# Kernel tuning notes

Measured on AMD Instinct MI355X. Metric: run time of the kernel, lower is better.

## Reference

```python
import jax, jax.numpy as jnp
import numpy as np

H = 1024        # hidden_size
E = 16          # n_routed_experts
K = 4           # num_experts_per_tok (top_k)
I = 512         # moe_intermediate_size
NS = 2          # n_shared_experts
IS = I * NS     # shared-expert intermediate size
N = 2048        # num_tokens
ROUTED_SCALE = 2.5  # routed_scaling_factor


def setup_inputs() -> dict:
    key = jax.random.key(0)
    ks = jax.random.split(key, 6)
    s = 0.02
    return {
        "hidden_states": jax.random.normal(ks[0], (N, H), jnp.float32),
        "gate_w": jax.random.normal(ks[1], (H, E), jnp.float32) * s,
        "w_gate_up": jax.random.normal(ks[2], (E, H, 2 * I), jnp.float32) * s,
        "w_down": jax.random.normal(ks[3], (E, I, H), jnp.float32) * s,
        "shared_gate_up": jax.random.normal(ks[4], (H, 2 * IS), jnp.float32) * s,
        "shared_down": jax.random.normal(ks[5], (IS, H), jnp.float32) * s,
    }


def _moe_forward(x, gate_w, w_gate_up, w_down, shared_gate_up, shared_down):
    n = x.shape[0]
    # --- router: sigmoid scoring + top-k (num_expert_group=topk_group=1) ---
    router_logits = x @ gate_w                      # [N, E]
    scores = jax.nn.sigmoid(router_logits)
    top_vals, top_idx = jax.lax.top_k(scores, K)    # [N, K]
    # renormalize (norm_topk_prob=True)
    top_w = top_vals / jnp.sum(top_vals, axis=-1, keepdims=True)
    # dense combine weights [N, E], zero outside top-k
    w_dense = jnp.zeros((n, E), x.dtype).at[jnp.arange(n)[:, None], top_idx].add(top_w)

    # --- routed experts: SwiGLU per expert, weighted combine ---
    gu = jnp.einsum("nh,ehf->nef", x, w_gate_up)    # [N, E, 2I]
    act = jax.nn.silu(gu[..., :I]) * gu[..., I:]    # SiluAndMul -> [N, E, I]
    routed = jnp.einsum("nei,eih,ne->nh", act, w_down, w_dense)  # [N, H]

    # --- shared experts MLP (WBLMLP) ---
    gus = x @ shared_gate_up                        # [N, 2*IS]
    shared = (jax.nn.silu(gus[:, :IS]) * gus[:, IS:]) @ shared_down  # [N, H]

    return routed * ROUTED_SCALE + shared


def reference(hidden_states, gate_w, w_gate_up, w_down, shared_gate_up, shared_down):
    return _moe_forward(hidden_states, gate_w, w_gate_up, w_down,
                        shared_gate_up, shared_down)
```

## Files before the change

### kernel.cpp

```cpp
#include <hip/hip_runtime.h>
#include <hip/hip_bf16.h>
#include <stdint.h>

#define NTOK 2048
#define HDIM 1024
#define NEXP 16
#define TOPK 4
#define IR   512
#define ISH  1024
#define RSCALE 2.5f

typedef short bf16x4 __attribute__((ext_vector_type(4)));
typedef short bf16x8 __attribute__((ext_vector_type(8)));
typedef float f32x4  __attribute__((ext_vector_type(4)));

static __device__ __forceinline__ unsigned short f2bf(float f){
  union { float fv; uint32_t u; } v; v.fv = f;
  uint32_t r = v.u + 0x7fffu + ((v.u >> 16) & 1u);
  return (unsigned short)(r >> 16);
}
static __device__ __forceinline__ float bf2f(unsigned short s){
  union { uint32_t u; float f; } v; v.u = ((uint32_t)s) << 16;
  return v.f;
}

static __device__ __forceinline__ void gl_lds16(const void* gp, void* lp){
  __builtin_amdgcn_global_load_lds(
      (const __attribute__((address_space(1))) unsigned int*)gp,
      (__attribute__((address_space(3))) unsigned int*)lp, 16, 0, 0);
}

__global__ __launch_bounds__(256) void router_kernel(
    const float* __restrict__ x, const float* __restrict__ gw,
    float* __restrict__ topkw, int* __restrict__ choice,
    unsigned short* __restrict__ xbf)
{
  __shared__ float sgw[NEXP][HDIM + 8];
  const int tid = threadIdx.x;
  for (int f = tid; f < HDIM * NEXP; f += 256){
    int i = f >> 4, e = f & 15;
    sgw[e][i] = gw[f];
  }
  __syncthreads();
  const int lane = tid & 63;
  const int t = blockIdx.x * 4 + (tid >> 6);

  float s[NEXP];
  #pragma unroll
  for (int e = 0; e < NEXP; e++) s[e] = 0.f;
  #pragma unroll
  for (int j = 0; j < 8; j++){
    const int off = 128 * j + lane * 2;
    float2 xv = *(const float2*)(x + (size_t)t * HDIM + off);
    ushort2 xs = { f2bf(xv.x), f2bf(xv.y) };
    *(ushort2*)(xbf + (size_t)t * HDIM + off) = xs;
    #pragma unroll
    for (int e = 0; e < NEXP; e++){
      float2 gv = *(const float2*)(&sgw[e][off]);
      s[e] += xv.x * gv.x + xv.y * gv.y;
    }
  }
  #pragma unroll
  for (int e = 0; e < NEXP; e++){
    #pragma unroll
    for (int off = 32; off; off >>= 1)
      s[e] += __shfl_xor(s[e], off);
  }
  float sc[NEXP];
  #pragma unroll
  for (int e = 0; e < NEXP; e++) sc[e] = 1.f / (1.f + __expf(-s[e]));

  unsigned mask = 0; float w[TOPK]; int id[TOPK];
  #pragma unroll
  for (int k = 0; k < TOPK; k++){
    float best = -1e30f; int bi = 0;
    #pragma unroll
    for (int e = 0; e < NEXP; e++){
      if (!((mask >> e) & 1u) && sc[e] > best){ best = sc[e]; bi = e; }
    }
    mask |= 1u << bi; id[k] = bi; w[k] = best;
  }
  float inv = 1.f / (w[0] + w[1] + w[2] + w[3]);
  if (lane == 0){
    #pragma unroll
    for (int k = 0; k < TOPK; k++){
      topkw[t * TOPK + k] = w[k] * inv;
      choice[t * TOPK + k] = id[k];
    }
  }
}

__global__ __launch_bounds__(256) void build_lists(
    const int* __restrict__ choice, int* __restrict__ counts, int* __restrict__ lists)
{
  const int e = blockIdx.x;
  const int tid = threadIdx.x;
  __shared__ int scnt[256];
  const int base = tid * 32;
  unsigned m = 0; int local = 0;
  #pragma unroll
  for (int i = 0; i < 32; i++){
    bool hit = (choice[base + i] == e);
    m |= (unsigned)hit << i;
    local += hit;
  }
  scnt[tid] = local;
  __syncthreads();
  int v = local;
  for (int off = 1; off < 256; off <<= 1){
    int add = (tid >= off) ? scnt[tid - off] : 0;
    __syncthreads();
    v += add; scnt[tid] = v;
    __syncthreads();
  }
  int pos = v - local;
  #pragma unroll
  for (int i = 0; i < 32; i++){
    if ((m >> i) & 1u) lists[e * NTOK + pos++] = base + i;
  }
  if (tid == 255) counts[e] = v;
}

__global__ __launch_bounds__(256) void gu_gemm(
    const unsigned short* __restrict__ xbf, const float* __restrict__ wgu,
    const float* __restrict__ sgu,
    unsigned short* __restrict__ act_r, unsigned short* __restrict__ act_s,
    const int* __restrict__ lists, const int* __restrict__ counts)
{
  __shared__ unsigned short sA[128 * 64];
  __shared__ unsigned short sB[128 * 64];
  __shared__ int sAid[128];

  const int tid = threadIdx.x;
  const int L = blockIdx.x;
  const bool routed = (L < 512);
  int e, mIdx, n0, count, NPAIR, NCH, LDB;
  const float* Bsrc;
  unsigned short* act;
  if (routed){
    e = L >> 5; int r = L & 31; mIdx = r >> 3; n0 = (r & 7) * 64;
    count = counts[e]; NPAIR = IR; NCH = 4; LDB = 2 * IR;
    Bsrc = wgu + (size_t)e * HDIM * (2 * IR);
    act = act_r;
  } else {
    int v = L - 512;
    e = 0; mIdx = v >> 4; n0 = (v & 15) * 64;
    count = NTOK; NPAIR = ISH; NCH = 16; LDB = 2 * ISH;
    Bsrc = sgu; act = act_s;
  }

  const int wv = tid >> 6, lane = tid & 63, lr = lane & 15, g = lane >> 4;
  const int wm = wv >> 1, wn = wv & 1;

  const int a = tid & 31, o = tid >> 5;
  const int alo = a & 15, aup = a >> 4;
  const int grp = ((alo >> 3) << 1) | aup;
  const int cbase = grp * 32 + 4 * (alo & 7);
  const int bsw = alo & 7;
  const int gcol = n0 + 4 * alo + (aup ? NPAIR : 0);
  const float* bthread = Bsrc + (size_t)(o * 8) * LDB + gcol;

  for (int mt = mIdx; mt * 128 < count; mt += NCH){
    const int m0 = mt * 128;
    __syncthreads();
    if (tid < 128){
      int idx = m0 + tid;
      int aid;
      if (routed) aid = (idx < count) ? lists[e * NTOK + idx] : lists[e * NTOK];
      else        aid = idx;
      sAid[tid] = aid;
    }
    __syncthreads();
    const unsigned short* asrc[4];
    #pragma unroll
    for (int it = 0; it < 4; it++){
      int s = tid + it * 256;
      int row = s >> 3, ch = s & 7;
      int aid = sAid[row];
      int tok = routed ? (aid >> 2) : aid;
      asrc[it] = xbf + (size_t)tok * HDIM + ch * 8;
    }

    const f32x4 z4 = {0.f, 0.f, 0.f, 0.f};
    f32x4 acc[4][4];
    #pragma unroll
    for (int i = 0; i < 4; i++)
      #pragma unroll
      for (int j = 0; j < 4; j++) acc[i][j] = z4;

    for (int k0 = 0; k0 < HDIM; k0 += 64){
      #pragma unroll
      for (int it = 0; it < 4; it++)
        gl_lds16(asrc[it] + k0, sA + (tid + it * 256) * 8);
      float4 f[8];
      const float* bp = bthread + (size_t)k0 * LDB;
      #pragma unroll
      for (int r = 0; r < 8; r++)
        f[r] = *(const float4*)(bp + (size_t)r * LDB);
      #pragma unroll
      for (int i = 0; i < 4; i++){
        const float* fp0 = (const float*)&f[0];
        bf16x8 pk = { (short)f2bf(((const float*)&f[0])[i]), (short)f2bf(((const float*)&f[1])[i]),
                      (short)f2bf(((const float*)&f[2])[i]), (short)f2bf(((const float*)&f[3])[i]),
                      (short)f2bf(((const float*)&f[4])[i]), (short)f2bf(((const float*)&f[5])[i]),
                      (short)f2bf(((const float*)&f[6])[i]), (short)f2bf(((const float*)&f[7])[i]) };
        (void)fp0;
        int c = cbase + i;
        *(bf16x8*)(sB + c * 64 + ((o ^ bsw) << 3)) = pk;
      }
      __syncthreads();
      #pragma unroll
      for (int h = 0; h < 2; h++){
        bf16x8 af[4], bfr[4];
        #pragma unroll
        for (int i = 0; i < 4; i++)
          af[i] = *(const bf16x8*)(sA + (wm * 64 + i * 16 + lr) * 64 + h * 32 + g * 8);
        #pragma unroll
        for (int i = 0; i < 4; i++){
          int c = wn * 64 + i * 16 + lr;
          int pos = (h * 4 + g) ^ ((c >> 2) & 7);
          bfr[i] = *(const bf16x8*)(sB + c * 64 + pos * 8);
        }
        #pragma unroll
        for (int mi = 0; mi < 4; mi++)
          #pragma unroll
          for (int ni = 0; ni < 4; ni++)
            acc[mi][ni] = __builtin_amdgcn_mfma_f32_16x16x32_bf16(af[mi], bfr[ni], acc[mi][ni], 0, 0, 0);
      }
      __syncthreads();
    }

    #pragma unroll
    for (int mi = 0; mi < 4; mi++){
      #pragma unroll
      for (int r = 0; r < 4; r++){
        int row = wm * 64 + mi * 16 + g * 4 + r;
        if (routed && m0 + row >= count) continue;
        int aid = sAid[row];
        size_t arow = (size_t)aid * NPAIR;
        #pragma unroll
        for (int ni = 0; ni < 2; ni++){
          float gv = acc[mi][ni][r];
          float uv = acc[mi][ni + 2][r];
          float av = gv / (1.f + __expf(-gv)) * uv;
          act[arow + n0 + wn * 32 + ni * 16 + lr] = f2bf(av);
        }
      }
    }
  }
}

__global__ __launch_bounds__(256) void down_gemm(
    const unsigned short* __restrict__ act_r, const unsigned short* __restrict__ act_s,
    const float* __restrict__ wdn, const float* __restrict__ sdn,
    float* __restrict__ out, unsigned short* __restrict__ downout,
    const int* __restrict__ lists, const int* __restrict__ counts)
{
  __shared__ unsigned short sA[128 * 64];
  __shared__ unsigned short sB[128 * 64];
  __shared__ int sAid[128];

  const int tid = threadIdx.x;
  const int L = blockIdx.x;
  const bool routed = (L < 512);
  int e, mIdx, n0, count, K, NCH;
  const float* Bsrc;
  const unsigned short* Ab;
  if (routed){
    e = L >> 5; int r = L & 31; mIdx = r >> 3; n0 = (r & 7) * 128;
    count = counts[e]; K = IR; NCH = 4;
    Bsrc = wdn + (size_t)e * IR * HDIM;
    Ab = act_r;
  } else {
    int v = L - 512;
    e = 0; mIdx = v >> 3; n0 = (v & 7) * 128;
    count = NTOK; K = ISH; NCH = 16;
    Bsrc = sdn; Ab = act_s;
  }

  const int wv = tid >> 6, lane = tid & 63, lr = lane & 15, g = lane >> 4;
  const int wm = wv >> 1, wn = wv & 1;

  const int a = tid & 31, o = tid >> 5;
  const int cbase = 4 * a;
  const int bsw = a & 7;
  const float* bthread = Bsrc + (size_t)(o * 8) * HDIM + n0 + 4 * a;

  for (int mt = mIdx; mt * 128 < count; mt += NCH){
    const int m0 = mt * 128;
    __syncthreads();
    if (tid < 128){
      int idx = m0 + tid;
      int aid;
      if (routed) aid = (idx < count) ? lists[e * NTOK + idx] : lists[e * NTOK];
      else        aid = idx;
      sAid[tid] = aid;
    }
    __syncthreads();
    const unsigned short* asrc[4];
    #pragma unroll
    for (int it = 0; it < 4; it++){
      int s = tid + it * 256;
      int row = s >> 3, ch = s & 7;
      asrc[it] = Ab + (size_t)sAid[row] * K + ch * 8;
    }

    const f32x4 z4 = {0.f, 0.f, 0.f, 0.f};
    f32x4 acc[4][4];
    #pragma unroll
    for (int i = 0; i < 4; i++)
      #pragma unroll
      for (int j = 0; j < 4; j++) acc[i][j] = z4;

    for (int k0 = 0; k0 < K; k0 += 64){
      #pragma unroll
      for (int it = 0; it < 4; it++)
        gl_lds16(asrc[it] + k0, sA + (tid + it * 256) * 8);
      float4 f[8];
      const float* bp = bthread + (size_t)k0 * HDIM;
      #pragma unroll
      for (int r = 0; r < 8; r++)
        f[r] = *(const float4*)(bp + (size_t)r * HDIM);
      #pragma unroll
      for (int i = 0; i < 4; i++){
        bf16x8 pk = { (short)f2bf(((const float*)&f[0])[i]), (short)f2bf(((const float*)&f[1])[i]),
                      (short)f2bf(((const float*)&f[2])[i]), (short)f2bf(((const float*)&f[3])[i]),
                      (short)f2bf(((const float*)&f[4])[i]), (short)f2bf(((const float*)&f[5])[i]),
                      (short)f2bf(((const float*)&f[6])[i]), (short)f2bf(((const float*)&f[7])[i]) };
        int c = cbase + i;
        *(bf16x8*)(sB + c * 64 + ((o ^ bsw) << 3)) = pk;
      }
      __syncthreads();
      #pragma unroll
      for (int h = 0; h < 2; h++){
        bf16x8 af[4], bfr[4];
        #pragma unroll
        for (int i = 0; i < 4; i++)
          af[i] = *(const bf16x8*)(sA + (wm * 64 + i * 16 + lr) * 64 + h * 32 + g * 8);
        #pragma unroll
        for (int i = 0; i < 4; i++){
          int c = wn * 64 + i * 16 + lr;
          int pos = (h * 4 + g) ^ ((c >> 2) & 7);
          bfr[i] = *(const bf16x8*)(sB + c * 64 + pos * 8);
        }
        #pragma unroll
        for (int mi = 0; mi < 4; mi++)
          #pragma unroll
          for (int ni = 0; ni < 4; ni++)
            acc[mi][ni] = __builtin_amdgcn_mfma_f32_16x16x32_bf16(af[mi], bfr[ni], acc[mi][ni], 0, 0, 0);
      }
      __syncthreads();
    }

    #pragma unroll
    for (int mi = 0; mi < 4; mi++){
      #pragma unroll
      for (int r = 0; r < 4; r++){
        int row = wm * 64 + mi * 16 + g * 4 + r;
        if (m0 + row >= count) continue;
        int aid = sAid[row];
        size_t orow = (size_t)aid * HDIM;
        if (routed){
          #pragma unroll
          for (int ni = 0; ni < 4; ni++)
            downout[orow + n0 + wn * 64 + ni * 16 + lr] = f2bf(acc[mi][ni][r]);
        } else {
          #pragma unroll
          for (int ni = 0; ni < 4; ni++)
            out[orow + n0 + wn * 64 + ni * 16 + lr] = acc[mi][ni][r];
        }
      }
    }
  }
}

__global__ __launch_bounds__(256) void combine_kernel(
    float* __restrict__ out, const unsigned short* __restrict__ downout,
    const float* __restrict__ topkw)
{
  const int idx = blockIdx.x * 256 + threadIdx.x;
  const int t = idx >> 8;
  const int c4 = (idx & 255) * 4;
  float4 o = *(float4*)(out + (size_t)t * HDIM + c4);
  float r0 = 0.f, r1 = 0.f, r2 = 0.f, r3 = 0.f;
  #pragma unroll
  for (int k = 0; k < TOPK; k++){
    float w = topkw[t * TOPK + k];
    const ushort4 dv = *(const ushort4*)(downout + (size_t)(t * TOPK + k) * HDIM + c4);
    r0 += w * bf2f(dv.x); r1 += w * bf2f(dv.y);
    r2 += w * bf2f(dv.z); r3 += w * bf2f(dv.w);
  }
  o.x += RSCALE * r0; o.y += RSCALE * r1; o.z += RSCALE * r2; o.w += RSCALE * r3;
  *(float4*)(out + (size_t)t * HDIM + c4) = o;
}

extern "C" void kernel_launch(void* const* d_in, const int* in_sizes, int n_in,
                              void* d_out, int out_size, void* d_ws, size_t ws_size,
                              hipStream_t stream) {
  const float* x   = (const float*)d_in[0];
  const float* gw  = (const float*)d_in[1];
  const float* wgu = (const float*)d_in[2];
  const float* wdn = (const float*)d_in[3];
  const float* sgu = (const float*)d_in[4];
  const float* sdn = (const float*)d_in[5];
  float* out = (float*)d_out;

  char* ws = (char*)d_ws;
  float* topkw = (float*)(ws + 0);
  int* choice  = (int*)(ws + 32768);
  int* counts  = (int*)(ws + 65536);
  int* lists   = (int*)(ws + 65792);
  unsigned short* xbf     = (unsigned short*)(ws + 197120);
  unsigned short* act_r   = (unsigned short*)(ws + 197120 +  4194304ull);
  unsigned short* act_s   = (unsigned short*)(ws + 197120 + 12582912ull);
  unsigned short* downout = (unsigned short*)(ws + 197120 + 16777216ull);

  router_kernel<<<NTOK / 4, 256, 0, stream>>>(x, gw, topkw, choice, xbf);
  build_lists<<<NEXP, 256, 0, stream>>>(choice, counts, lists);
  gu_gemm<<<768, 256, 0, stream>>>(xbf, wgu, sgu, act_r, act_s, lists, counts);
  down_gemm<<<640, 256, 0, stream>>>(act_r, act_s, wdn, sdn, out, downout, lists, counts);
  combine_kernel<<<(NTOK * HDIM / 4) / 256, 256, 0, stream>>>(out, downout, topkw);
}
```

Measured before the change: 141.5 us.

## Replace LDS-direct loads with register staging and XOR-swizzled LDS layout

```diff
diff --git a/kernel.cpp b/kernel.cpp
--- a/kernel.cpp
+++ b/kernel.cpp
@@ -23,11 +23,10 @@
   union { uint32_t u; float f; } v; v.u = ((uint32_t)s) << 16;
   return v.f;
 }
-
-static __device__ __forceinline__ void gl_lds16(const void* gp, void* lp){
-  __builtin_amdgcn_global_load_lds(
-      (const __attribute__((address_space(1))) unsigned int*)gp,
-      (__attribute__((address_space(3))) unsigned int*)lp, 16, 0, 0);
+static __device__ __forceinline__ unsigned int pkbf2(float lo, float hi){
+  union { __hip_bfloat162 b; unsigned int u; } cv;
+  cv.b = __float22bfloat162_rn(make_float2(lo, hi));
+  return cv.u;
 }
 
 __global__ __launch_bounds__(256) void router_kernel(
@@ -151,12 +150,12 @@
 
   const int wv = tid >> 6, lane = tid & 63, lr = lane & 15, g = lane >> 4;
   const int wm = wv >> 1, wn = wv & 1;
+  const int sw = lr >> 1;
 
   const int a = tid & 31, o = tid >> 5;
   const int alo = a & 15, aup = a >> 4;
   const int grp = ((alo >> 3) << 1) | aup;
   const int cbase = grp * 32 + 4 * (alo & 7);
-  const int bsw = alo & 7;
   const int gcol = n0 + 4 * alo + (aup ? NPAIR : 0);
   const float* bthread = Bsrc + (size_t)(o * 8) * LDB + gcol;
 
@@ -172,13 +171,15 @@
     }
     __syncthreads();
     const unsigned short* asrc[4];
+    unsigned short* adst[4];
     #pragma unroll
     for (int it = 0; it < 4; it++){
       int s = tid + it * 256;
-      int row = s >> 3, ch = s & 7;
+      int row = s >> 3, j = s & 7;
       int aid = sAid[row];
       int tok = routed ? (aid >> 2) : aid;
-      asrc[it] = xbf + (size_t)tok * HDIM + ch * 8;
+      asrc[it] = xbf + (size_t)tok * HDIM + j * 8;
+      adst[it] = sA + row * 64 + (j ^ ((row >> 1) & 7)) * 8;
     }
 
     const f32x4 z4 = {0.f, 0.f, 0.f, 0.f};
@@ -189,9 +190,13 @@
       for (int j = 0; j < 4; j++) acc[i][j] = z4;
 
     for (int k0 = 0; k0 < HDIM; k0 += 64){
+      bf16x8 av[4];
       #pragma unroll
       for (int it = 0; it < 4; it++)
-        gl_lds16(asrc[it] + k0, sA + (tid + it * 256) * 8);
+        av[it] = *(const bf16x8*)(asrc[it] + k0);
+      #pragma unroll
+      for (int it = 0; it < 4; it++)
+        *(bf16x8*)adst[it] = av[it];
       float4 f[8];
       const float* bp = bthread + (size_t)k0 * LDB;
       #pragma unroll
@@ -199,27 +204,26 @@
         f[r] = *(const float4*)(bp + (size_t)r * LDB);
       #pragma unroll
       for (int i = 0; i < 4; i++){
-        const float* fp0 = (const float*)&f[0];
-        bf16x8 pk = { (short)f2bf(((const float*)&f[0])[i]), (short)f2bf(((const float*)&f[1])[i]),
-                      (short)f2bf(((const float*)&f[2])[i]), (short)f2bf(((const float*)&f[3])[i]),
-                      (short)f2bf(((const float*)&f[4])[i]), (short)f2bf(((const float*)&f[5])[i]),
-                      (short)f2bf(((const float*)&f[6])[i]), (short)f2bf(((const float*)&f[7])[i]) };
-        (void)fp0;
+        union { bf16x8 v; unsigned int u[4]; } pk;
+        #pragma unroll
+        for (int rp = 0; rp < 4; rp++){
+          float lo = ((const float*)&f[2 * rp    ])[i];
+          float hi = ((const float*)&f[2 * rp + 1])[i];
+          pk.u[rp] = pkbf2(lo, hi);
+        }
         int c = cbase + i;
-        *(bf16x8*)(sB + c * 64 + ((o ^ bsw) << 3)) = pk;
+        int pos = o ^ ((c >> 1) & 7);
+        *(bf16x8*)(sB + c * 64 + pos * 8) = pk.v;
       }
       __syncthreads();
       #pragma unroll
       for (int h = 0; h < 2; h++){
         bf16x8 af[4], bfr[4];
         #pragma unroll
-        for (int i = 0; i < 4; i++)
-          af[i] = *(const bf16x8*)(sA + (wm * 64 + i * 16 + lr) * 64 + h * 32 + g * 8);
-        #pragma unroll
         for (int i = 0; i < 4; i++){
-          int c = wn * 64 + i * 16 + lr;
-          int pos = (h * 4 + g) ^ ((c >> 2) & 7);
-          bfr[i] = *(const bf16x8*)(sB + c * 64 + pos * 8);
+          int jx = ((h * 4 + g) ^ sw) * 8;
+          af[i]  = *(const bf16x8*)(sA + (wm * 64 + i * 16 + lr) * 64 + jx);
+          bfr[i] = *(const bf16x8*)(sB + (wn * 64 + i * 16 + lr) * 64 + jx);
         }
         #pragma unroll
         for (int mi = 0; mi < 4; mi++)
@@ -242,8 +246,8 @@
         for (int ni = 0; ni < 2; ni++){
           float gv = acc[mi][ni][r];
           float uv = acc[mi][ni + 2][r];
-          float av = gv / (1.f + __expf(-gv)) * uv;
-          act[arow + n0 + wn * 32 + ni * 16 + lr] = f2bf(av);
+          float av2 = gv / (1.f + __expf(-gv)) * uv;
+          act[arow + n0 + wn * 32 + ni * 16 + lr] = f2bf(av2);
         }
       }
     }
@@ -253,7 +257,7 @@
 __global__ __launch_bounds__(256) void down_gemm(
     const unsigned short* __restrict__ act_r, const unsigned short* __restrict__ act_s,
     const float* __restrict__ wdn, const float* __restrict__ sdn,
-    float* __restrict__ out, unsigned short* __restrict__ downout,
+    float* __restrict__ shout, unsigned short* __restrict__ downout,
     const int* __restrict__ lists, const int* __restrict__ counts)
 {
   __shared__ unsigned short sA[128 * 64];
@@ -280,10 +284,10 @@
 
   const int wv = tid >> 6, lane = tid & 63, lr = lane & 15, g = lane >> 4;
   const int wm = wv >> 1, wn = wv & 1;
+  const int sw = lr >> 1;
 
   const int a = tid & 31, o = tid >> 5;
   const int cbase = 4 * a;
-  const int bsw = a & 7;
   const float* bthread = Bsrc + (size_t)(o * 8) * HDIM + n0 + 4 * a;
 
   for (int mt = mIdx; mt * 128 < count; mt += NCH){
@@ -298,11 +302,13 @@
     }
     __syncthreads();
     const unsigned short* asrc[4];
+    unsigned short* adst[4];
     #pragma unroll
     for (int it = 0; it < 4; it++){
       int s = tid + it * 256;
-      int row = s >> 3, ch = s & 7;
-      asrc[it] = Ab + (size_t)sAid[row] * K + ch * 8;
+      int row = s >> 3, j = s & 7;
+      asrc[it] = Ab + (size_t)sAid[row] * K + j * 8;
+      adst[it] = sA + row * 64 + (j ^ ((row >> 1) & 7)) * 8;
     }
 
     const f32x4 z4 = {0.f, 0.f, 0.f, 0.f};
@@ -313,9 +319,13 @@
       for (int j = 0; j < 4; j++) acc[i][j] = z4;
 
     for (int k0 = 0; k0 < K; k0 += 64){
+      bf16x8 av[4];
       #pragma unroll
       for (int it = 0; it < 4; it++)
-        gl_lds16(asrc[it] + k0, sA + (tid + it * 256) * 8);
+        av[it] = *(const bf16x8*)(asrc[it] + k0);
+      #pragma unroll
+      for (int it = 0; it < 4; it++)
+        *(bf16x8*)adst[it] = av[it];
       float4 f[8];
       const float* bp = bthread + (size_t)k0 * HDIM;
       #pragma unroll
@@ -323,25 +333,26 @@
         f[r] = *(const float4*)(bp + (size_t)r * HDIM);
       #pragma unroll
       for (int i = 0; i < 4; i++){
-        bf16x8 pk = { (short)f2bf(((const float*)&f[0])[i]), (short)f2bf(((const float*)&f[1])[i]),
-                      (short)f2bf(((const float*)&f[2])[i]), (short)f2bf(((const float*)&f[3])[i]),
-                      (short)f2bf(((const float*)&f[4])[i]), (short)f2bf(((const float*)&f[5])[i]),
-                      (short)f2bf(((const float*)&f[6])[i]), (short)f2bf(((const float*)&f[7])[i]) };
+        union { bf16x8 v; unsigned int u[4]; } pk;
+        #pragma unroll
+        for (int rp = 0; rp < 4; rp++){
+          float lo = ((const float*)&f[2 * rp    ])[i];
+          float hi = ((const float*)&f[2 * rp + 1])[i];
+          pk.u[rp] = pkbf2(lo, hi);
+        }
         int c = cbase + i;
-        *(bf16x8*)(sB + c * 64 + ((o ^ bsw) << 3)) = pk;
+        int pos = o ^ ((c >> 1) & 7);
+        *(bf16x8*)(sB + c * 64 + pos * 8) = pk.v;
       }
       __syncthreads();
       #pragma unroll
       for (int h = 0; h < 2; h++){
         bf16x8 af[4], bfr[4];
         #pragma unroll
-        for (int i = 0; i < 4; i++)
-          af[i] = *(const bf16x8*)(sA + (wm * 64 + i * 16 + lr) * 64 + h * 32 + g * 8);
-        #pragma unroll
         for (int i = 0; i < 4; i++){
-          int c = wn * 64 + i * 16 + lr;
-          int pos = (h * 4 + g) ^ ((c >> 2) & 7);
-          bfr[i] = *(const bf16x8*)(sB + c * 64 + pos * 8);
+          int jx = ((h * 4 + g) ^ sw) * 8;
+          af[i]  = *(const bf16x8*)(sA + (wm * 64 + i * 16 + lr) * 64 + jx);
+          bfr[i] = *(const bf16x8*)(sB + (wn * 64 + i * 16 + lr) * 64 + jx);
         }
         #pragma unroll
         for (int mi = 0; mi < 4; mi++)
@@ -367,7 +378,7 @@
         } else {
           #pragma unroll
           for (int ni = 0; ni < 4; ni++)
-            out[orow + n0 + wn * 64 + ni * 16 + lr] = acc[mi][ni][r];
+            shout[orow + n0 + wn * 64 + ni * 16 + lr] = acc[mi][ni][r];
         }
       }
     }
@@ -375,13 +386,13 @@
 }
 
 __global__ __launch_bounds__(256) void combine_kernel(
-    float* __restrict__ out, const unsigned short* __restrict__ downout,
-    const float* __restrict__ topkw)
+    float* __restrict__ out, const float* __restrict__ shout,
+    const unsigned short* __restrict__ downout, const float* __restrict__ topkw)
 {
   const int idx = blockIdx.x * 256 + threadIdx.x;
   const int t = idx >> 8;
   const int c4 = (idx & 255) * 4;
-  float4 o = *(float4*)(out + (size_t)t * HDIM + c4);
+  float4 o = *(const float4*)(shout + (size_t)t * HDIM + c4);
   float r0 = 0.f, r1 = 0.f, r2 = 0.f, r3 = 0.f;
   #pragma unroll
   for (int k = 0; k < TOPK; k++){
@@ -414,10 +425,11 @@
   unsigned short* act_r   = (unsigned short*)(ws + 197120 +  4194304ull);
   unsigned short* act_s   = (unsigned short*)(ws + 197120 + 12582912ull);
   unsigned short* downout = (unsigned short*)(ws + 197120 + 16777216ull);
+  float*          shout   = (float*)(ws + 197120 + 33554432ull);
 
   router_kernel<<<NTOK / 4, 256, 0, stream>>>(x, gw, topkw, choice, xbf);
   build_lists<<<NEXP, 256, 0, stream>>>(choice, counts, lists);
   gu_gemm<<<768, 256, 0, stream>>>(xbf, wgu, sgu, act_r, act_s, lists, counts);
-  down_gemm<<<640, 256, 0, stream>>>(act_r, act_s, wdn, sdn, out, downout, lists, counts);
-  combine_kernel<<<(NTOK * HDIM / 4) / 256, 256, 0, stream>>>(out, downout, topkw);
-}
+  down_gemm<<<640, 256, 0, stream>>>(act_r, act_s, wdn, sdn, shout, downout, lists, counts);
+  combine_kernel<<<(NTOK * HDIM / 4) / 256, 256, 0, stream>>>(out, shout, downout, topkw);
+}
```

Result: faster. 130.4 us (-7.9%).
